# Kernel optimization log

Hardware: AMD Instinct MI355X
Metric: run time of the kernel (lower is better)

Reference implementation:

```python
import jax, jax.numpy as jnp
import numpy as np

N_EMBD = 1024
N_HEAD = 16
HEAD_SIZE = N_EMBD // N_HEAD
BLOCK_SIZE = 2048
B, T = 2, 2048
EPS = 1e-5


def _layernorm(x, g, b):
    mu = jnp.mean(x, axis=-1, keepdims=True)
    var = jnp.mean(jnp.square(x - mu), axis=-1, keepdims=True)
    return (x - mu) * jax.lax.rsqrt(var + EPS) * g + b


def setup_inputs() -> dict:
    key = jax.random.key(0)
    ks = jax.random.split(key, 12)
    s = 0.02
    x = jax.random.normal(ks[0], (B, T, N_EMBD), dtype=jnp.float32)
    wq = jax.random.normal(ks[1], (N_HEAD, N_EMBD, HEAD_SIZE), jnp.float32) * s
    wk = jax.random.normal(ks[2], (N_HEAD, N_EMBD, HEAD_SIZE), jnp.float32) * s
    wv = jax.random.normal(ks[3], (N_HEAD, N_EMBD, HEAD_SIZE), jnp.float32) * s
    w_proj = jax.random.normal(ks[4], (N_EMBD, N_EMBD), jnp.float32) * s
    b_proj = jnp.zeros((N_EMBD,), jnp.float32)
    w1 = jax.random.normal(ks[5], (N_EMBD, 4 * N_EMBD), jnp.float32) * s
    b1 = jnp.zeros((4 * N_EMBD,), jnp.float32)
    w2 = jax.random.normal(ks[6], (4 * N_EMBD, N_EMBD), jnp.float32) * s
    b2 = jnp.zeros((N_EMBD,), jnp.float32)
    g1 = jnp.ones((N_EMBD,), jnp.float32)
    be1 = jnp.zeros((N_EMBD,), jnp.float32)
    g2 = jnp.ones((N_EMBD,), jnp.float32)
    be2 = jnp.zeros((N_EMBD,), jnp.float32)
    return dict(x=x, wq=wq, wk=wk, wv=wv, w_proj=w_proj, b_proj=b_proj,
                w1=w1, b1=b1, w2=w2, b2=b2, g1=g1, be1=be1, g2=g2, be2=be2)


def reference(x, wq, wk, wv, w_proj, b_proj, w1, b1, w2, b2, g1, be1, g2, be2):
    # --- self-attention with pre-LN ---
    h = _layernorm(x, g1, be1)
    q = jnp.einsum('btc,hcd->bhtd', h, wq)
    k = jnp.einsum('btc,hcd->bhtd', h, wk)
    v = jnp.einsum('btc,hcd->bhtd', h, wv)
    scores = jnp.einsum('bhtd,bhsd->bhts', q, k) / np.sqrt(HEAD_SIZE).astype(np.float32)
    causal = jnp.tril(jnp.ones((T, T), dtype=bool))
    scores = jnp.where(causal, scores, -jnp.inf)
    weights = jax.nn.softmax(scores, axis=-1)
    attn = jnp.einsum('bhts,bhsd->bhtd', weights, v)  # (B,H,T,D)
    attn = attn.transpose(0, 2, 1, 3).reshape(B, T, N_EMBD)  # concat heads
    sa = attn @ w_proj + b_proj
    x = x + sa
    # --- feed-forward with pre-LN ---
    h2 = _layernorm(x, g2, be2)
    ff = jax.nn.relu(h2 @ w1 + b1) @ w2 + b2
    return x + ff
```

## Files before the change

### kernel.cpp

```cpp
#include <hip/hip_runtime.h>
#include <hip/hip_bf16.h>
#include <cstdint>


typedef unsigned short u16;
typedef __attribute__((ext_vector_type(8))) __bf16 bf16x8;
typedef __attribute__((ext_vector_type(4))) float f32x4;

__device__ __forceinline__ float b2f(u16 v) {
    union { float f; unsigned int u; } x; x.u = ((unsigned int)v) << 16; return x.f;
}
__device__ __forceinline__ u16 f2b(float f) {
    union { float f; unsigned int u; } x; x.f = f;
    unsigned int u = x.u;
    u += 0x7fffu + ((u >> 16) & 1u);
    return (u16)(u >> 16);
}

__device__ __forceinline__ f32x4 mfma16(bf16x8 a, bf16x8 b, f32x4 c) {
    return __builtin_amdgcn_mfma_f32_16x16x32_bf16(a, b, c, 0, 0, 0);
}

__device__ __forceinline__ void load_lds16(const u16* g, u16* l) {
    __builtin_amdgcn_global_load_lds(
        (const __attribute__((address_space(1))) unsigned int*)g,
        (__attribute__((address_space(3))) unsigned int*)l, 16, 0, 0);
}

__global__ __launch_bounds__(256) void transpose_f2b(
    const float* __restrict__ src, u16* __restrict__ dst, int R, int C)
{
    __shared__ float tile[32][33];
    const int b = blockIdx.z;
    src += (size_t)b * R * C;
    dst += (size_t)b * R * C;
    const int tx = threadIdx.x;
    const int ty = threadIdx.y;
    const int c0 = blockIdx.x * 32, r0 = blockIdx.y * 32;
#pragma unroll
    for (int i = 0; i < 4; ++i) {
        int r = ty * 4 + i;
        tile[r][tx] = src[(size_t)(r0 + r) * C + c0 + tx];
    }
    __syncthreads();
#pragma unroll
    for (int i = 0; i < 4; ++i) {
        int r = ty * 4 + i;
        dst[(size_t)(c0 + r) * R + r0 + tx] = f2b(tile[tx][r]);
    }
}

__global__ __launch_bounds__(256) void ln_kernel(
    const float* __restrict__ x, const float* __restrict__ g,
    const float* __restrict__ be, u16* __restrict__ out)
{
    const int row = blockIdx.x;
    const int tid = threadIdx.x;
    const float* xr = x + (size_t)row * 1024;
    float v[4];
#pragma unroll
    for (int i = 0; i < 4; ++i) v[i] = xr[tid + i * 256];
    float s = v[0] + v[1] + v[2] + v[3];
    float q = v[0]*v[0] + v[1]*v[1] + v[2]*v[2] + v[3]*v[3];
#pragma unroll
    for (int o = 1; o < 64; o <<= 1) {
        s += __shfl_xor(s, o, 64);
        q += __shfl_xor(q, o, 64);
    }
    __shared__ float red[8];
    const int wave = tid >> 6;
    if ((tid & 63) == 0) { red[wave] = s; red[4 + wave] = q; }
    __syncthreads();
    s = red[0] + red[1] + red[2] + red[3];
    q = red[4] + red[5] + red[6] + red[7];
    const float mu = s * (1.0f / 1024.0f);
    const float var = q * (1.0f / 1024.0f) - mu * mu;
    const float rstd = rsqrtf(var + 1e-5f);
#pragma unroll
    for (int i = 0; i < 4; ++i) {
        int idx = tid + i * 256;
        out[(size_t)row * 1024 + idx] = f2b((v[i] - mu) * rstd * g[idx] + be[idx]);
    }
}

template <int EPI, int TM, int TN, int WM, int WN>
__global__ __launch_bounds__(256, 2) void gemm_bt(
    const u16* __restrict__ A, const u16* __restrict__ Bt,
    int M, int N, int K,
    const float* __restrict__ bias, const float* __restrict__ resid_f,
    u16* __restrict__ out_b, float* __restrict__ out_f)
{
    constexpr int MI = WM / 16, NI = WN / 16;
    constexpr int MWAVES = TM / WM;
    __shared__ alignas(16) u16 As[TM * 32];
    __shared__ alignas(16) u16 Bs[TN * 32];
    const int tid = threadIdx.x;
    const int wave = tid >> 6, lane = tid & 63;
    const int lr = lane >> 4, lc = lane & 15;
    const int m0 = blockIdx.x * TM, n0 = blockIdx.y * TN;
    const int wm = (wave % MWAVES) * WM, wn = (wave / MWAVES) * WN;

    f32x4 acc[MI][NI];
#pragma unroll
    for (int i = 0; i < MI; ++i)
#pragma unroll
        for (int j = 0; j < NI; ++j) acc[i][j] = (f32x4){0.f, 0.f, 0.f, 0.f};

    const int stgrow = wave * 16 + (lane >> 2);
    const int sdb = (lane & 3) ^ ((lane >> 3) & 3);
    const u16* Agp = A + (size_t)(m0 + stgrow) * K + sdb * 8;
    const u16* Bgp = Bt + (size_t)(n0 + stgrow) * K + sdb * 8;
    const int qread = (lr ^ ((lc >> 1) & 3)) * 8;

    for (int k0 = 0; k0 < K; k0 += 32) {
#pragma unroll
        for (int i = 0; i < TM / 64; ++i)
            load_lds16(Agp + (size_t)i * 64 * K + k0, As + i * 2048 + wave * 512);
#pragma unroll
        for (int i = 0; i < TN / 64; ++i)
            load_lds16(Bgp + (size_t)i * 64 * K + k0, Bs + i * 2048 + wave * 512);
        __syncthreads();
        bf16x8 af[MI], bfr[NI];
#pragma unroll
        for (int i = 0; i < MI; ++i)
            af[i] = *(const bf16x8*)&As[(wm + i * 16 + lc) * 32 + qread];
#pragma unroll
        for (int j = 0; j < NI; ++j)
            bfr[j] = *(const bf16x8*)&Bs[(wn + j * 16 + lc) * 32 + qread];
#pragma unroll
        for (int i = 0; i < MI; ++i)
#pragma unroll
            for (int j = 0; j < NI; ++j)
                acc[i][j] = mfma16(af[i], bfr[j], acc[i][j]);
        __syncthreads();
    }

#pragma unroll
    for (int i = 0; i < MI; ++i) {
#pragma unroll
        for (int j = 0; j < NI; ++j) {
#pragma unroll
            for (int r = 0; r < 4; ++r) {
                const int m = m0 + wm + i * 16 + lr * 4 + r;
                const int n = n0 + wn + j * 16 + lc;
                const float v = acc[i][j][r];
                if (EPI == 0) {
                    const int group = n >> 10, nn = n & 1023;
                    const int hh = nn >> 6, dd = nn & 63;
                    const int bb = m >> 11, tt = m & 2047;
                    if (group == 0)
                        out_b[(((size_t)(bb * 16 + hh) * 2048) + tt) * 64 + dd] =
                            f2b(v * 0.125f);
                    else if (group == 1)
                        out_b[4194304u + (((size_t)(bb * 16 + hh) * 2048) + tt) * 64 + dd] =
                            f2b(v);
                    else
                        out_b[8388608u + (((size_t)(bb * 16 + hh) * 64) + dd) * 2048 + tt] =
                            f2b(v);
                } else if (EPI == 4) {
                    size_t idx = (size_t)m * N + n;
                    float rv = v + bias[n];
                    out_b[idx] = f2b(rv > 0.f ? rv : 0.f);
                } else {
                    size_t idx = (size_t)m * N + n;
                    out_f[idx] = resid_f[idx] + v + bias[n];
                }
            }
        }
    }
}

__global__ __launch_bounds__(256) void attn_kernel(
    const u16* __restrict__ qb, const u16* __restrict__ kb,
    const u16* __restrict__ vtb, u16* __restrict__ ob)
{
    const int bh = blockIdx.y;
    const int b = bh >> 4, h = bh & 15;
    const int tid = threadIdx.x, wave = tid >> 6, lane = tid & 63;
    const int lr = lane >> 4, lc = lane & 15;
    const int qx = lc & 7;
    __shared__ alignas(16) u16 Ks[64 * 64];
    __shared__ alignas(16) u16 Vts[64 * 64];
    __shared__ alignas(16) u16 Ps[4][16 * 64];
    const size_t base = (size_t)bh * (2048 * 64);

    const int srow = lane >> 3;
    const int sdb = (lane & 7) ^ srow;
    const u16* kg0 = kb + base + (size_t)(wave * 16 + srow) * 64 + sdb * 8;
    const u16* vg0 = vtb + base + (size_t)(wave * 16 + srow) * 2048 + sdb * 8;
    u16* KsW = Ks + wave * 16 * 64;
    u16* VsW = Vts + wave * 16 * 64;
    const int q0 = (lr ^ qx) * 8;
    const int q1 = ((4 + lr) ^ qx) * 8;

    for (int half = 0; half < 2; ++half) {
        const int qt = half ? (31 - (int)blockIdx.x) : (int)blockIdx.x;
        const int t0 = qt * 64;
        const int trow = t0 + wave * 16 + lc;
        const bf16x8 qf0 = *(const bf16x8*)&qb[base + (size_t)trow * 64 + lr * 8];
        const bf16x8 qf1 = *(const bf16x8*)&qb[base + (size_t)trow * 64 + 32 + lr * 8];
        f32x4 O[4];
        float pls[4];
#pragma unroll
        for (int j = 0; j < 4; ++j) O[j] = (f32x4){0.f, 0.f, 0.f, 0.f};
#pragma unroll
        for (int r = 0; r < 4; ++r) pls[r] = 0.f;

        for (int c = 0; c <= qt; ++c) {
            const int s0 = c * 64;
            load_lds16(kg0 + (size_t)s0 * 64, KsW);
            load_lds16(kg0 + (size_t)s0 * 64 + 512, KsW + 512);
            load_lds16(vg0 + s0, VsW);
            load_lds16(vg0 + s0 + 8 * 2048, VsW + 512);
            __syncthreads();

            f32x4 sc[4];
#pragma unroll
            for (int j = 0; j < 4; ++j) sc[j] = (f32x4){0.f, 0.f, 0.f, 0.f};
#pragma unroll
            for (int j = 0; j < 4; ++j) {
                const int row = (j * 16 + lc) * 64;
                bf16x8 k0 = *(const bf16x8*)&Ks[row + q0];
                bf16x8 k1 = *(const bf16x8*)&Ks[row + q1];
                sc[j] = mfma16(qf0, k0, sc[j]);
                sc[j] = mfma16(qf1, k1, sc[j]);
            }
            const bool diag = (c == qt);
#pragma unroll
            for (int r = 0; r < 4; ++r) {
                const int tl = lr * 4 + r;
#pragma unroll
                for (int j = 0; j < 4; ++j) {
                    float pv = __expf(sc[j][r]);
                    if (diag && (j * 16 + lc > wave * 16 + tl)) pv = 0.f;
                    pls[r] += pv;
                    const int sb = j * 2 + (lc >> 3);
                    Ps[wave][tl * 64 + ((sb ^ (tl & 7)) * 8) + (lc & 7)] = f2b(pv);
                }
            }
            const bf16x8 pf0 = *(const bf16x8*)&Ps[wave][lc * 64 + q0];
            const bf16x8 pf1 = *(const bf16x8*)&Ps[wave][lc * 64 + q1];
#pragma unroll
            for (int j = 0; j < 4; ++j) {
                const int row = (j * 16 + lc) * 64;
                bf16x8 v0 = *(const bf16x8*)&Vts[row + q0];
                bf16x8 v1 = *(const bf16x8*)&Vts[row + q1];
                O[j] = mfma16(pf0, v0, O[j]);
                O[j] = mfma16(pf1, v1, O[j]);
            }
            __syncthreads();
        }

        float linv[4];
#pragma unroll
        for (int r = 0; r < 4; ++r) {
            float l = pls[r];
            l += __shfl_xor(l, 1, 64);
            l += __shfl_xor(l, 2, 64);
            l += __shfl_xor(l, 4, 64);
            l += __shfl_xor(l, 8, 64);
            linv[r] = 1.0f / l;
        }
#pragma unroll
        for (int j = 0; j < 4; ++j)
#pragma unroll
            for (int r = 0; r < 4; ++r) {
                const int tr = t0 + wave * 16 + lr * 4 + r;
                ob[((size_t)b * 2048 + tr) * 1024 + h * 64 + j * 16 + lc] =
                    f2b(O[j][r] * linv[r]);
            }
    }
}

extern "C" void kernel_launch(void* const* d_in, const int* in_sizes, int n_in,
                              void* d_out, int out_size, void* d_ws, size_t ws_size,
                              hipStream_t stream)
{
    (void)in_sizes; (void)n_in; (void)out_size; (void)ws_size;
    const float* x   = (const float*)d_in[0];
    const float* wq  = (const float*)d_in[1];
    const float* wk  = (const float*)d_in[2];
    const float* wv  = (const float*)d_in[3];
    const float* wp  = (const float*)d_in[4];
    const float* bp  = (const float*)d_in[5];
    const float* w1  = (const float*)d_in[6];
    const float* b1  = (const float*)d_in[7];
    const float* w2  = (const float*)d_in[8];
    const float* b2  = (const float*)d_in[9];
    const float* g1  = (const float*)d_in[10];
    const float* be1 = (const float*)d_in[11];
    const float* g2  = (const float*)d_in[12];
    const float* be2 = (const float*)d_in[13];
    float* out = (float*)d_out;

    char* ws = (char*)d_ws;
    const size_t MB = 1024ull * 1024;
    u16*   h1    = (u16*)(ws + 0);
    u16*   wqkvt = (u16*)(ws + 8 * MB);
    u16*   wpt   = (u16*)(ws + 14 * MB);
    u16*   w1t   = (u16*)(ws + 16 * MB);
    u16*   w2t   = (u16*)(ws + 24 * MB);
    u16*   qkv   = (u16*)(ws + 32 * MB);
    u16*   attnb = (u16*)(ws + 56 * MB);
    u16*   ff1   = (u16*)(ws + 32 * MB);
    float* x2    = (float*)(ws + 64 * MB);
    u16*   h2    = h1;
    u16*   qb    = qkv;
    u16*   kbf   = qkv + 4194304u;
    u16*   vtb   = qkv + 8388608u;

    const dim3 tb(32, 8);
    transpose_f2b<<<dim3(2, 32, 16), tb, 0, stream>>>(wq, wqkvt, 1024, 64);
    transpose_f2b<<<dim3(2, 32, 16), tb, 0, stream>>>(wk, wqkvt + 1048576u, 1024, 64);
    transpose_f2b<<<dim3(2, 32, 16), tb, 0, stream>>>(wv, wqkvt + 2097152u, 1024, 64);
    transpose_f2b<<<dim3(32, 32, 1), tb, 0, stream>>>(wp, wpt, 1024, 1024);
    transpose_f2b<<<dim3(128, 32, 1), tb, 0, stream>>>(w1, w1t, 1024, 4096);
    transpose_f2b<<<dim3(32, 128, 1), tb, 0, stream>>>(w2, w2t, 4096, 1024);

    ln_kernel<<<4096, 256, 0, stream>>>(x, g1, be1, h1);

    gemm_bt<0, 128, 128, 64, 64><<<dim3(32, 24), 256, 0, stream>>>(
        h1, wqkvt, 4096, 3072, 1024, nullptr, nullptr, qkv, nullptr);

    attn_kernel<<<dim3(16, 32), 256, 0, stream>>>(qb, kbf, vtb, attnb);

    gemm_bt<3, 64, 128, 32, 64><<<dim3(64, 8), 256, 0, stream>>>(
        attnb, wpt, 4096, 1024, 1024, bp, x, nullptr, x2);

    ln_kernel<<<4096, 256, 0, stream>>>(x2, g2, be2, h2);

    gemm_bt<4, 128, 128, 64, 64><<<dim3(32, 32), 256, 0, stream>>>(
        h2, w1t, 4096, 4096, 1024, b1, nullptr, ff1, nullptr);

    gemm_bt<5, 64, 128, 32, 64><<<dim3(64, 8), 256, 0, stream>>>(
        ff1, w2t, 4096, 1024, 4096, b2, x2, nullptr, out);
}
```

Before: 368.0 us.

## Deepen GEMM K-tile to 64 with new LDS swizzle; merge weight transposes into one launch

The GEMM main loop now stages a K-slice of 64 instead of 32 per iteration. It uses a new 8-way XOR swizzle for LDS staging and reads, and does two MFMA sub-steps per sync. This halves the number of barrier pairs and loop iterations per GEMM at the cost of doubled LDS per block, which may reduce occupancy. Separately, the six weight transpose/convert launches are fused into one kernel that dispatches on block index, cutting launch overhead.

```diff
diff --git a/kernel.cpp b/kernel.cpp
--- a/kernel.cpp
+++ b/kernel.cpp
@@ -27,16 +27,36 @@
         (__attribute__((address_space(3))) unsigned int*)l, 16, 0, 0);
 }
 
-__global__ __launch_bounds__(256) void transpose_f2b(
-    const float* __restrict__ src, u16* __restrict__ dst, int R, int C)
+__global__ __launch_bounds__(256) void transpose_all(
+    const float* __restrict__ wq, const float* __restrict__ wk,
+    const float* __restrict__ wv, const float* __restrict__ wp,
+    const float* __restrict__ w1, const float* __restrict__ w2,
+    u16* __restrict__ wqkvt, u16* __restrict__ wpt,
+    u16* __restrict__ w1t, u16* __restrict__ w2t)
 {
     __shared__ float tile[32][33];
-    const int b = blockIdx.z;
-    src += (size_t)b * R * C;
-    dst += (size_t)b * R * C;
-    const int tx = threadIdx.x;
-    const int ty = threadIdx.y;
-    const int c0 = blockIdx.x * 32, r0 = blockIdx.y * 32;
+    int id = blockIdx.x;
+    const float* src; u16* dst; int R, C, bx, by;
+    if (id < 3072) {
+        const int m = id >> 10;
+        src = (m == 0) ? wq : (m == 1) ? wk : wv;
+        dst = wqkvt + m * 1048576u;
+        int t = id & 1023;
+        const int b = t >> 6; t &= 63;
+        R = 1024; C = 64; bx = t & 1; by = t >> 1;
+        src += (size_t)b * 65536; dst += (size_t)b * 65536;
+    } else if (id < 4096) {
+        int t = id - 3072; src = wp; dst = wpt;
+        R = 1024; C = 1024; bx = t & 31; by = t >> 5;
+    } else if (id < 8192) {
+        int t = id - 4096; src = w1; dst = w1t;
+        R = 1024; C = 4096; bx = t & 127; by = t >> 7;
+    } else {
+        int t = id - 8192; src = w2; dst = w2t;
+        R = 4096; C = 1024; bx = t & 31; by = t >> 5;
+    }
+    const int tx = threadIdx.x, ty = threadIdx.y;
+    const int c0 = bx * 32, r0 = by * 32;
 #pragma unroll
     for (int i = 0; i < 4; ++i) {
         int r = ty * 4 + i;
@@ -92,8 +112,8 @@
 {
     constexpr int MI = WM / 16, NI = WN / 16;
     constexpr int MWAVES = TM / WM;
-    __shared__ alignas(16) u16 As[TM * 32];
-    __shared__ alignas(16) u16 Bs[TN * 32];
+    __shared__ alignas(16) u16 As[TM * 64];
+    __shared__ alignas(16) u16 Bs[TN * 64];
     const int tid = threadIdx.x;
     const int wave = tid >> 6, lane = tid & 63;
     const int lr = lane >> 4, lc = lane & 15;
@@ -106,32 +126,36 @@
 #pragma unroll
         for (int j = 0; j < NI; ++j) acc[i][j] = (f32x4){0.f, 0.f, 0.f, 0.f};
 
-    const int stgrow = wave * 16 + (lane >> 2);
-    const int sdb = (lane & 3) ^ ((lane >> 3) & 3);
-    const u16* Agp = A + (size_t)(m0 + stgrow) * K + sdb * 8;
-    const u16* Bgp = Bt + (size_t)(n0 + stgrow) * K + sdb * 8;
-    const int qread = (lr ^ ((lc >> 1) & 3)) * 8;
-
-    for (int k0 = 0; k0 < K; k0 += 32) {
-#pragma unroll
-        for (int i = 0; i < TM / 64; ++i)
-            load_lds16(Agp + (size_t)i * 64 * K + k0, As + i * 2048 + wave * 512);
-#pragma unroll
-        for (int i = 0; i < TN / 64; ++i)
-            load_lds16(Bgp + (size_t)i * 64 * K + k0, Bs + i * 2048 + wave * 512);
+    const int srow = lane >> 3;
+    const int skb = (lane & 7) ^ srow;
+    const u16* Agp = A + (size_t)(m0 + wave * 8 + srow) * K + skb * 8;
+    const u16* Bgp = Bt + (size_t)(n0 + wave * 8 + srow) * K + skb * 8;
+    const int ldst = wave * 512;
+
+    for (int k0 = 0; k0 < K; k0 += 64) {
+#pragma unroll
+        for (int i = 0; i < TM / 32; ++i)
+            load_lds16(Agp + (size_t)i * 32 * K + k0, As + i * 2048 + ldst);
+#pragma unroll
+        for (int i = 0; i < TN / 32; ++i)
+            load_lds16(Bgp + (size_t)i * 32 * K + k0, Bs + i * 2048 + ldst);
         __syncthreads();
-        bf16x8 af[MI], bfr[NI];
-#pragma unroll
-        for (int i = 0; i < MI; ++i)
-            af[i] = *(const bf16x8*)&As[(wm + i * 16 + lc) * 32 + qread];
-#pragma unroll
-        for (int j = 0; j < NI; ++j)
-            bfr[j] = *(const bf16x8*)&Bs[(wn + j * 16 + lc) * 32 + qread];
-#pragma unroll
-        for (int i = 0; i < MI; ++i)
+#pragma unroll
+        for (int h = 0; h < 2; ++h) {
+            const int qh = ((h * 4 + lr) ^ (lc & 7)) * 8;
+            bf16x8 af[MI], bfr[NI];
+#pragma unroll
+            for (int i = 0; i < MI; ++i)
+                af[i] = *(const bf16x8*)&As[(wm + i * 16 + lc) * 64 + qh];
 #pragma unroll
             for (int j = 0; j < NI; ++j)
-                acc[i][j] = mfma16(af[i], bfr[j], acc[i][j]);
+                bfr[j] = *(const bf16x8*)&Bs[(wn + j * 16 + lc) * 64 + qh];
+#pragma unroll
+            for (int i = 0; i < MI; ++i)
+#pragma unroll
+                for (int j = 0; j < NI; ++j)
+                    acc[i][j] = mfma16(af[i], bfr[j], acc[i][j]);
+        }
         __syncthreads();
     }
 
@@ -309,13 +333,8 @@
     u16*   kbf   = qkv + 4194304u;
     u16*   vtb   = qkv + 8388608u;
 
-    const dim3 tb(32, 8);
-    transpose_f2b<<<dim3(2, 32, 16), tb, 0, stream>>>(wq, wqkvt, 1024, 64);
-    transpose_f2b<<<dim3(2, 32, 16), tb, 0, stream>>>(wk, wqkvt + 1048576u, 1024, 64);
-    transpose_f2b<<<dim3(2, 32, 16), tb, 0, stream>>>(wv, wqkvt + 2097152u, 1024, 64);
-    transpose_f2b<<<dim3(32, 32, 1), tb, 0, stream>>>(wp, wpt, 1024, 1024);
-    transpose_f2b<<<dim3(128, 32, 1), tb, 0, stream>>>(w1, w1t, 1024, 4096);
-    transpose_f2b<<<dim3(32, 128, 1), tb, 0, stream>>>(w2, w2t, 4096, 1024);
+    transpose_all<<<12288, dim3(32, 8), 0, stream>>>(
+        wq, wk, wv, wp, w1, w2, wqkvt, wpt, w1t, w2t);
 
     ln_kernel<<<4096, 256, 0, stream>>>(x, g1, be1, h1);
 
```

New measurement: 340.1 us. 1.08x faster.
